# Kernel tuning notes

Measured on AMD Instinct MI355X. Metric: run time of the kernel, lower is better.

Reference implementation:

```python
import jax, jax.numpy as jnp
import numpy as np

DIM = 2048            # model dim
HID = 4096            # ssm inner dim (multiple_of*round(2/3*6144))
H = 64                # n_heads
P = HID // H          # head_dim = 64
N = 128               # state_dim
G = 1                 # n_groups
K = 4                 # conv_size
Q = 128               # chunk_size
CONV_DIM = HID + 2 * G * N       # 4352
D_IN = 2 * HID + 2 * G * N + H   # 8512
EPS = 1e-5


def _causal_conv_silu(xBC, w):
    # xBC: [B,L,C], w: [C,K]; depthwise causal conv1d fused with SiLU
    kern = w.T[:, None, :]  # [K,1,C]
    y = jax.lax.conv_general_dilated(
        xBC, kern, window_strides=(1,), padding=[(K - 1, 0)],
        dimension_numbers=('NHC', 'HIO', 'NHC'),
        feature_group_count=xBC.shape[-1])
    return y * jax.nn.sigmoid(y)


def _ssm(x, W_in, conv_w, dt_bias, A_log, D, norm_w, W_out):
    Bsz, L, _ = x.shape
    zxbcdt = x @ W_in.T                       # [B,L,D_IN]
    z = zxbcdt[..., :HID]                     # gate
    xBC = zxbcdt[..., HID:HID + CONV_DIM]
    dt_raw = zxbcdt[..., HID + CONV_DIM:]     # [B,L,H]

    xBC = _causal_conv_silu(xBC, conv_w)
    xs = xBC[..., :HID].reshape(Bsz, L, H, P)
    rep = H // G
    Bh = jnp.repeat(xBC[..., HID:HID + G * N].reshape(Bsz, L, G, N), rep, axis=2)  # [B,L,H,N]
    Ch = jnp.repeat(xBC[..., HID + G * N:].reshape(Bsz, L, G, N), rep, axis=2)

    dt = jax.nn.softplus(dt_raw + dt_bias)    # [B,L,H], dt_softplus=True
    A = -jnp.exp(A_log)                       # [H]

    # ---- chunked selective scan (Mamba2 SSD), chunk size Q ----
    nc = L // Q
    a = (dt * A).reshape(Bsz, nc, Q, H)
    cum = jnp.cumsum(a, axis=2)               # inclusive within-chunk cumsum, <= 0
    xs_c = xs.reshape(Bsz, nc, Q, H, P)
    dtc = dt.reshape(Bsz, nc, Q, H)
    Bc = Bh.reshape(Bsz, nc, Q, H, N)
    Cc = Ch.reshape(Bsz, nc, Q, H, N)

    # intra-chunk (diagonal) part: Y[i] += sum_{j<=i} exp(cum_i-cum_j) dt_j (C_i.B_j) x_j
    diff = cum[:, :, :, None, :] - cum[:, :, None, :, :]     # [b,c,i,j,h]
    tril = jnp.tril(jnp.ones((Q, Q), bool))[None, None, :, :, None]
    Lmat = jnp.exp(jnp.where(tril, diff, -jnp.inf))          # causal decay matrix
    CB = jnp.einsum('bcihn,bcjhn->bcijh', Cc, Bc)
    M = CB * Lmat * dtc[:, :, None, :, :]
    Yd = jnp.einsum('bcijh,bcjhp->bcihp', M, xs_c)

    # per-chunk end state: sum_j exp(cum_last-cum_j) dt_j x_j (x) B_j
    wdec = jnp.exp(cum[:, :, -1:, :] - cum) * dtc            # [b,c,q,h]
    states = jnp.einsum('bcqh,bcqhn,bcqhp->bchpn', wdec, Bc, xs_c)
    chunk_decay = jnp.exp(cum[:, :, -1, :])                  # [b,c,h]

    # inter-chunk recurrence over nc chunks
    def step(S, inp):
        dec, st = inp                                        # [b,h], [b,h,p,n]
        return S * dec[..., None, None] + st, S              # emit state entering chunk
    S0 = jnp.zeros((Bsz, H, P, N), x.dtype)
    _, Sprev = jax.lax.scan(step, S0,
                            (chunk_decay.transpose(1, 0, 2),
                             states.transpose(1, 0, 2, 3, 4)))
    Sprev = Sprev.transpose(1, 0, 2, 3, 4)                   # [b,c,h,p,n]

    # inter-chunk (off-diagonal) contribution
    Yoff = jnp.einsum('bcqh,bcqhn,bchpn->bcqhp', jnp.exp(cum), Cc, Sprev)

    y = (Yd + Yoff).reshape(Bsz, L, H, P) + D[None, None, :, None] * xs  # skip D
    y = y.reshape(Bsz, L, HID)

    yz = y * (z * jax.nn.sigmoid(z))                         # gated: y * silu(z)
    yn = yz * jax.lax.rsqrt(jnp.mean(yz * yz, axis=-1, keepdims=True) + EPS) * norm_w
    return yn @ W_out.T


def setup_inputs() -> dict:
    key = jax.random.key(0)
    k = jax.random.split(key, 6)
    return {
        'x': jax.random.normal(k[0], (2, 4096, DIM), jnp.float32),
        'W_in': jax.random.normal(k[1], (D_IN, DIM), jnp.float32) * DIM ** -0.5,
        'conv_w': jax.random.normal(k[2], (CONV_DIM, K), jnp.float32) * K ** -0.5,
        'dt_bias': jax.random.uniform(k[3], (H,), jnp.float32, minval=0.001, maxval=0.1),
        'A_log': jnp.log(jax.random.uniform(k[4], (H,), jnp.float32, minval=1.0, maxval=16.0)),
        'D': jnp.ones((H,), jnp.float32),
        'norm_w': jnp.ones((HID,), jnp.float32),
        'W_out': jax.random.normal(k[5], (DIM, HID), jnp.float32) * HID ** -0.5,
    }


def reference(x, W_in, conv_w, dt_bias, A_log, D, norm_w, W_out):
    return _ssm(x, W_in, conv_w, dt_bias, A_log, D, norm_w, W_out)
```

## Files before the change

### kernel.cpp

```cpp
#include <hip/hip_runtime.h>
#include <hip/hip_fp16.h>
#include <math.h>

#define ROWS   8192
#define DIMK   2048
#define HIDN   4096
#define QCH    128
#define NCHUNK 32
#define CST    136
#define RST    68

typedef __attribute__((ext_vector_type(8))) short short8;
typedef __attribute__((ext_vector_type(8))) _Float16 half8;
typedef __attribute__((ext_vector_type(4))) float floatx4;

static __device__ inline unsigned short f2h(float f){
  union { _Float16 h; unsigned short u; } v; v.h = (_Float16)f; return v.u;
}
static __device__ inline float h2f(unsigned short u){
  union { unsigned short u; _Float16 h; } v; v.u = u; return (float)v.h;
}
static __device__ inline void async_cp16(const void* g, void* l){
  __builtin_amdgcn_global_load_lds((const __attribute__((address_space(1))) void*)g,
                                   (__attribute__((address_space(3))) void*)l, 16, 0, 0);
}

__global__ void k_prep(const float* __restrict__ x, const float* __restrict__ Win,
                       const float* __restrict__ Wout, unsigned short* __restrict__ xw,
                       unsigned short* __restrict__ winb, unsigned short* __restrict__ woutb){
  int blk = blockIdx.x, t = threadIdx.x;
  const float* src; unsigned short* dst; int i;
  if (blk < 16384){ src = x;    dst = xw;    i = blk * 256 + t; }
  else if (blk < 33280){ src = Win;  dst = winb;  i = (blk - 16384) * 256 + t; }
  else { src = Wout; dst = woutb; i = (blk - 33280) * 256 + t; }
  float4 v = ((const float4*)src)[i];
  unsigned long long p = (unsigned long long)f2h(v.x)
                       | ((unsigned long long)f2h(v.y) << 16)
                       | ((unsigned long long)f2h(v.z) << 32)
                       | ((unsigned long long)f2h(v.w) << 48);
  ((unsigned long long*)dst)[i] = p;
}

#define DT_KT 128
__global__ __launch_bounds__(256)
void k_dtraw(const float* __restrict__ x, const float* __restrict__ Win,
             float* __restrict__ dtraw){
  __shared__ float ws[64 * (DT_KT + 4)];
  const int t = threadIdx.x;
  const int lane = t & 63, w = t >> 6;
  const int r0 = blockIdx.x * 8;
  const int rw = __builtin_amdgcn_readfirstlane(r0 + w * 2);
  float acc0 = 0.f, acc1 = 0.f;
  for (int k0 = 0; k0 < DIMK; k0 += DT_KT){
    __syncthreads();
#pragma unroll
    for (int l = 0; l < 8; l++){
      int fidx = (l * 256 + t) * 4;
      int row = fidx >> 7, col = fidx & 127;
      *(float4*)&ws[row * 132 + col] =
          *(const float4*)&Win[(size_t)(8448 + row) * DIMK + k0 + col];
    }
    __syncthreads();
    const float* xa = x + (size_t)rw * DIMK + k0;
    const float* xb = xa + DIMK;
#pragma unroll 8
    for (int kk = 0; kk < DT_KT; kk += 4){
      float4 wv = *(const float4*)&ws[lane * 132 + kk];
      float4 va = *(const float4*)&xa[kk];
      float4 vb = *(const float4*)&xb[kk];
      acc0 += wv.x*va.x + wv.y*va.y + wv.z*va.z + wv.w*va.w;
      acc1 += wv.x*vb.x + wv.y*vb.y + wv.z*vb.z + wv.w*vb.w;
    }
  }
  dtraw[(size_t)rw * 64 + lane]       = acc0;
  dtraw[(size_t)(rw + 1) * 64 + lane] = acc1;
}

static __device__ inline unsigned ldsaddr(const void* p){
  return (unsigned)(size_t)(const __attribute__((address_space(3))) void*)p;
}
static __device__ inline floatx4 dsr128(unsigned a){
  floatx4 d;
  asm volatile("ds_read_b128 %0, %1" : "=v"(d) : "v"(a));
  return d;
}
static __device__ inline half8 as_h8(floatx4 f){
  union { floatx4 f; half8 h; } u; u.f = f; return u.h;
}

template<int KD>
__device__ inline void gemm256_core(const unsigned short* __restrict__ A,
                                    const unsigned short* __restrict__ B,
                                    int row0, int col0,
                                    unsigned short* sA, unsigned short* sB,
                                    floatx4 (&acc)[8][4], int t){
  const int lane = t & 63, wid = t >> 6;
  const int wm = wid >> 2, wn = wid & 3;
  const int quad = lane >> 4, l16 = lane & 15;
  const int srow  = t >> 3;
  const int sslot = (t & 7) ^ (srow & 7);
  constexpr int NT = KD / 64;

  auto stageA = [&](int d, int half, int kt){
    unsigned short* dst = sA + d*256*64 + half*128*64;
    const unsigned short* src = A + (size_t)(row0 + half*128) * KD + kt*64;
#pragma unroll
    for (int i = 0; i < 2; i++)
      async_cp16(src + (size_t)(i*64 + srow) * KD + sslot*8,
                 dst + ((size_t)i*512 + t)*8);
  };
  auto stageB = [&](int d, int half, int kt){
    unsigned short* dst = sB + d*256*64 + half*128*64;
    const unsigned short* src = B + (size_t)(col0 + half*128) * KD + kt*64;
#pragma unroll
    for (int i = 0; i < 2; i++)
      async_cp16(src + (size_t)(i*64 + srow) * KD + sslot*8,
                 dst + ((size_t)i*512 + t)*8);
  };

  const unsigned sAbase = ldsaddr(sA), sBbase = ldsaddr(sB);
  floatx4 af[8][2], bf[4][2];
  auto rdA = [&](unsigned base, int fr, int ks) -> floatx4 {
    return dsr128(base + 2u*(unsigned)((fr*16 + l16)*64 + (((ks*4+quad)^(l16&7))*8)));
  };
  auto rdB = [&](unsigned base, int fc, int ks) -> floatx4 {
    return dsr128(base + 2u*(unsigned)((fc*16 + l16)*64 + (((ks*4+quad)^(l16&7))*8)));
  };
  auto mmac = [&](int mh, int nh){
    __builtin_amdgcn_s_setprio(1);
#pragma unroll
    for (int mm = 0; mm < 4; mm++)
#pragma unroll
      for (int nn = 0; nn < 2; nn++)
#pragma unroll
        for (int ks = 0; ks < 2; ks++)
          acc[mh*4+mm][nh*2+nn] = __builtin_amdgcn_mfma_f32_16x16x32_f16(
              as_h8(af[mh*4+mm][ks]), as_h8(bf[nh*2+nn][ks]), acc[mh*4+mm][nh*2+nn], 0, 0, 0);
    __builtin_amdgcn_s_setprio(0);
  };

  stageA(0,0,0); stageA(0,1,0); stageB(0,0,0); stageB(0,1,0);
  stageA(1,0,1); stageA(1,1,1);
  asm volatile("s_waitcnt vmcnt(4)" ::: "memory");
  __builtin_amdgcn_s_barrier();

  for (int T = 0; T < NT; T++){
    const int cur = T & 1;
    const unsigned aAd = sAbase + 2u*(unsigned)(cur*256*64 + wm*128*64);
    const unsigned bAd = sBbase + 2u*(unsigned)(cur*256*64 + wn*64*64);
#pragma unroll
    for (int fr = 0; fr < 4; fr++)
#pragma unroll
      for (int ks = 0; ks < 2; ks++)
        af[fr][ks] = rdA(aAd, fr, ks);
#pragma unroll
    for (int fc = 0; fc < 2; fc++)
#pragma unroll
      for (int ks = 0; ks < 2; ks++)
        bf[fc][ks] = rdB(bAd, fc, ks);
    if (T + 1 < NT) stageB(cur^1, 0, T+1);
    __builtin_amdgcn_s_barrier();
    asm volatile("s_waitcnt lgkmcnt(0)" ::: "memory");
    __builtin_amdgcn_sched_barrier(0);
    mmac(0, 0);
    __builtin_amdgcn_s_barrier();
#pragma unroll
    for (int fr = 4; fr < 8; fr++)
#pragma unroll
      for (int ks = 0; ks < 2; ks++)
        af[fr][ks] = rdA(aAd, fr, ks);
    if (T + 1 < NT) stageB(cur^1, 1, T+1);
    __builtin_amdgcn_s_barrier();
    asm volatile("s_waitcnt lgkmcnt(0)" ::: "memory");
    __builtin_amdgcn_sched_barrier(0);
    mmac(1, 0);
    __builtin_amdgcn_s_barrier();
#pragma unroll
    for (int fc = 2; fc < 4; fc++)
#pragma unroll
      for (int ks = 0; ks < 2; ks++)
        bf[fc][ks] = rdB(bAd, fc, ks);
    __builtin_amdgcn_s_barrier();
    asm volatile("s_waitcnt lgkmcnt(0)" ::: "memory");
    __builtin_amdgcn_sched_barrier(0);
    mmac(0, 1);
    __builtin_amdgcn_s_barrier();
    if (T + 2 < NT){
      stageA(cur, 0, T+2); stageA(cur, 1, T+2);
      asm volatile("s_waitcnt vmcnt(4)" ::: "memory");
    } else if (T + 1 < NT){
      asm volatile("s_waitcnt vmcnt(0)" ::: "memory");
    }
    __builtin_amdgcn_s_barrier();
    mmac(1, 1);
    __builtin_amdgcn_s_barrier();
  }
}

__global__ __launch_bounds__(512, 2)
void k_gemm1(const unsigned short* __restrict__ A, const unsigned short* __restrict__ B,
             unsigned short* __restrict__ zbuf, unsigned short* __restrict__ xsraw,
             unsigned short* __restrict__ bcraw){
  __shared__ __align__(16) unsigned short sA[2*256*64];
  __shared__ __align__(16) unsigned short sB[2*256*64];
  const int t = threadIdx.x;
  int swz = (blockIdx.x % 8) * 132 + blockIdx.x / 8;
  const int row0 = (swz & 31) * 256, col0 = (swz >> 5) * 256;
  floatx4 acc[8][4] = {};
  gemm256_core<DIMK>(A, B, row0, col0, sA, sB, acc, t);
  const int lane = t & 63, wid = t >> 6;
  const int wm = wid >> 2, wn = wid & 3;
  const int quad = lane >> 4, l16 = lane & 15;
  unsigned short* dst; int cbase, ldd;
  if (col0 < 4096){ dst = zbuf; cbase = 0; ldd = 4096; }
  else if (col0 < 8192){ dst = xsraw; cbase = 4096; ldd = 4096; }
  else { dst = bcraw; cbase = 8192; ldd = 256; }
#pragma unroll
  for (int m = 0; m < 8; m++)
#pragma unroll
    for (int n = 0; n < 4; n++){
      int rb = row0 + wm*128 + m*16 + quad*4;
      int cc = col0 + wn*64 + n*16 + l16 - cbase;
#pragma unroll
      for (int r = 0; r < 4; r++)
        dst[(size_t)(rb + r) * ldd + cc] = f2h(acc[m][n][r]);
    }
}

__global__ __launch_bounds__(512, 2)
void k_gemm2(const unsigned short* __restrict__ A, const unsigned short* __restrict__ B,
             float* __restrict__ C){
  __shared__ __align__(16) unsigned short sA[2*256*64];
  __shared__ __align__(16) unsigned short sB[2*256*64];
  const int t = threadIdx.x;
  int swz = (blockIdx.x % 8) * 32 + blockIdx.x / 8;
  const int row0 = (swz & 31) * 256, col0 = (swz >> 5) * 256;
  floatx4 acc[8][4] = {};
  gemm256_core<HIDN>(A, B, row0, col0, sA, sB, acc, t);
  const int lane = t & 63, wid = t >> 6;
  const int wm = wid >> 2, wn = wid & 3;
  const int quad = lane >> 4, l16 = lane & 15;
#pragma unroll
  for (int m = 0; m < 8; m++)
#pragma unroll
    for (int n = 0; n < 4; n++){
      int rb = row0 + wm*128 + m*16 + quad*4;
      int cc = col0 + wn*64 + n*16 + l16;
#pragma unroll
      for (int r = 0; r < 4; r++)
        C[(size_t)(rb + r) * DIMK + cc] = acc[m][n][r];
    }
}

__global__ void k_mid(const unsigned short* __restrict__ bcraw, const float* __restrict__ cw,
                      unsigned short* __restrict__ bcc,
                      const unsigned short* __restrict__ xsraw, unsigned short* __restrict__ halo,
                      const float* __restrict__ dtraw, const float* __restrict__ dtbias,
                      const float* __restrict__ Alog, float* __restrict__ dtb,
                      float* __restrict__ cumb){
  int blk = blockIdx.x, t = threadIdx.x;
  if (blk < 8192){
    int row = blk, c = t;
    int tl = row & 4095;
    const float4 wv = *(const float4*)&cw[(size_t)(4096 + c) * 4];
    const unsigned short* col = bcraw + c;
    size_t rb = (size_t)row * 256;
    float a = h2f(col[rb]) * wv.w;
    if (tl >= 1) a += h2f(col[rb - 256]) * wv.z;
    if (tl >= 2) a += h2f(col[rb - 512]) * wv.y;
    if (tl >= 3) a += h2f(col[rb - 768]) * wv.x;
    bcc[rb + c] = f2h(a / (1.f + __expf(-a)));
  } else if (blk < 11264){
    int idx = blk - 8192;
    int col = (idx & 15) * 256 + t;
    int slot = (idx >> 4) % 3;
    int bc = idx / 48;
    long r = (long)bc * QCH - 3 + slot;
    if (r >= 0)
      halo[((size_t)bc * 3 + slot) * 4096 + col] = xsraw[(size_t)r * 4096 + col];
  } else {
    int lb = blk - 11264;
    int bc = lb * 4 + (t >> 6);
    int h = t & 63;
    float bias = dtbias[h];
    float A = -__expf(Alog[h]);
    float run = 0.f;
    size_t rowb = (size_t)bc * QCH;
    for (int q = 0; q < QCH; q++){
      float dr = dtraw[(rowb + q) * 64 + h] + bias;
      float dt = dr > 20.f ? dr : log1pf(__expf(dr));
      dtb[(rowb + q) * 64 + h] = dt;
      run += dt * A;
      cumb[(rowb + q) * 64 + h] = run;
    }
  }
}

__global__ __launch_bounds__(256, 2)
void k_chunk1(const unsigned short* __restrict__ xsc, const unsigned short* __restrict__ bcc,
              const float* __restrict__ dtb, const float* __restrict__ cumb,
              const float* __restrict__ Dp, const unsigned short* __restrict__ st,
              unsigned short* __restrict__ ybuf){
  __shared__ __align__(16) unsigned short Ml[128*CST];
  __shared__ __align__(16) unsigned short xsT[64*CST];
  __shared__ float cum_s[128], dt_s[128];
  const int blk = blockIdx.x, h = blk & 63, bc = blk >> 6;
  const size_t rowb = (size_t)bc * QCH;
  const int t = threadIdx.x, w = t >> 6, lane = t & 63, quad = lane >> 4, l16 = lane & 15;
  const int wrow = w * 32;
  if (t < 128){ cum_s[t] = cumb[(rowb + t)*64 + h]; dt_s[t] = dtb[(rowb + t)*64 + h]; }
  __syncthreads();
#pragma unroll
  for (int it = 0; it < 2; it++){
    int idx = it * 256 + t;
    int q = idx & 127, p0 = (idx >> 7) * 16;
    const unsigned short* cur = xsc + (rowb + q) * 4096 + h * 64 + p0;
    short8 c0 = *(const short8*)cur, c1 = *(const short8*)(cur + 8);
#pragma unroll
    for (int j = 0; j < 16; j++)
      xsT[(p0 + j) * CST + q] = (unsigned short)(j < 8 ? c0[j] : c1[j-8]);
  }
  floatx4 acc[2][8] = {};
  const unsigned short* Cb = bcc + rowb * 256 + 128;
  const unsigned short* Bb = bcc + rowb * 256;
#pragma unroll
  for (int ks = 0; ks < 4; ks++){
    half8 af[2];
#pragma unroll
    for (int i = 0; i < 2; i++)
      af[i] = *(const half8*)(Cb + (size_t)(wrow + i*16 + l16) * 256 + ks*32 + quad*8);
#pragma unroll
    for (int j = 0; j < 8; j++){
      half8 bfr = *(const half8*)(Bb + (size_t)(j*16 + l16) * 256 + ks*32 + quad*8);
#pragma unroll
      for (int i = 0; i < 2; i++)
        acc[i][j] = __builtin_amdgcn_mfma_f32_16x16x32_f16(af[i], bfr, acc[i][j], 0, 0, 0);
    }
  }
#pragma unroll
  for (int i = 0; i < 2; i++)
#pragma unroll
    for (int j = 0; j < 8; j++){
      int jc = j*16 + l16;
      float dtj = dt_s[jc], cj = cum_s[jc];
#pragma unroll
      for (int r = 0; r < 4; r++){
        int ir = wrow + i*16 + quad*4 + r;
        float m = (ir >= jc) ? acc[i][j][r] * __expf(cum_s[ir] - cj) * dtj : 0.f;
        Ml[ir * CST + jc] = f2h(m);
      }
    }
  __syncthreads();
  floatx4 accY[2][4] = {};
#pragma unroll
  for (int ks = 0; ks < 4; ks++){
    half8 af[2], bfr[4];
#pragma unroll
    for (int i = 0; i < 2; i++)
      af[i] = *(const half8*)&Ml[(wrow + i*16 + l16)*CST + ks*32 + quad*8];
#pragma unroll
    for (int p = 0; p < 4; p++)
      bfr[p] = *(const half8*)&xsT[(p*16 + l16)*CST + ks*32 + quad*8];
#pragma unroll
    for (int i = 0; i < 2; i++)
#pragma unroll
      for (int p = 0; p < 4; p++)
        accY[i][p] = __builtin_amdgcn_mfma_f32_16x16x32_f16(af[i], bfr[p], accY[i][p], 0, 0, 0);
  }
  __syncthreads();
  unsigned short* Sp = Ml;
  {
    size_t base = ((size_t)bc * 64 + h) * 8192;
#pragma unroll
    for (int it = 0; it < 4; it++){
      int flat = it * 256 + t;
      int row = flat >> 4, col = (flat & 15) * 8;
      *(short8*)&Sp[row * CST + col] = *(const short8*)&st[base + (size_t)row * 128 + col];
    }
  }
  __syncthreads();
  floatx4 accO[2][4] = {};
#pragma unroll
  for (int ks = 0; ks < 4; ks++){
    half8 af[2], bfr[4];
#pragma unroll
    for (int i = 0; i < 2; i++)
      af[i] = *(const half8*)(Cb + (size_t)(wrow + i*16 + l16) * 256 + ks*32 + quad*8);
#pragma unroll
    for (int p = 0; p < 4; p++)
      bfr[p] = *(const half8*)&Sp[(p*16 + l16)*CST + ks*32 + quad*8];
#pragma unroll
    for (int i = 0; i < 2; i++)
#pragma unroll
      for (int p = 0; p < 4; p++)
        accO[i][p] = __builtin_amdgcn_mfma_f32_16x16x32_f16(af[i], bfr[p], accO[i][p], 0, 0, 0);
  }
  float Dh = Dp[h];
#pragma unroll
  for (int i = 0; i < 2; i++)
#pragma unroll
    for (int p = 0; p < 4; p++){
      int pc = p*16 + l16;
#pragma unroll
      for (int r = 0; r < 4; r++){
        int ir = wrow + i*16 + quad*4 + r;
        float y = accY[i][p][r] + __expf(cum_s[ir]) * accO[i][p][r] + Dh * h2f(xsT[pc*CST + ir]);
        ybuf[(rowb + ir) * (size_t)HIDN + h*64 + pc] = f2h(y);
      }
    }
}

__global__ __launch_bounds__(256, 2)
void k_chunk2(unsigned short* __restrict__ xsraw, const unsigned short* __restrict__ bcc,
              const unsigned short* __restrict__ halo, const float* __restrict__ cw,
              const float* __restrict__ dtb, const float* __restrict__ cumb,
              unsigned short* __restrict__ st){
  __shared__ __align__(16) unsigned short wBT[128*CST];
  __shared__ __align__(16) unsigned short xsT[64*CST];
  __shared__ __align__(16) unsigned short xsRaw[131*RST];
  __shared__ float cum_s[128], dt_s[128];
  __shared__ float cws[64*4];
  const int blk = blockIdx.x, h = blk & 63, bc = blk >> 6;
  const size_t rowb = (size_t)bc * QCH;
  const int t = threadIdx.x, w = t >> 6, lane = t & 63, quad = lane >> 4, l16 = lane & 15;
  if (t < 128){ cum_s[t] = cumb[(rowb + t)*64 + h]; dt_s[t] = dtb[(rowb + t)*64 + h]; }
  if (t < 64) *(float4*)&cws[t*4] = *(const float4*)&cw[((size_t)h*64 + t)*4];
#pragma unroll
  for (int it = 0; it < 5; it++){
    int flat = it * 256 + t;
    if (flat < 1048){
      int row = flat >> 3, c8 = (flat & 7) * 8;
      const unsigned short* src = (row < 3)
        ? halo + ((size_t)bc * 3 + row) * 4096 + h * 64 + c8
        : xsraw + (rowb + row - 3) * 4096 + h * 64 + c8;
      *(short8*)&xsRaw[row * RST + c8] = *(const short8*)src;
    }
  }
  __syncthreads();
  const int tl0 = (bc & 31) * QCH;
#pragma unroll
  for (int it = 0; it < 2; it++){
    int idx = it * 256 + t;
    int q = idx & 127, p0 = (idx >> 7) * 16;
    int tl = tl0 + q;
    int lr = q + 3;
    float f1 = (tl >= 1) ? 1.f : 0.f;
    float f2 = (tl >= 2) ? 1.f : 0.f;
    float f3 = (tl >= 3) ? 1.f : 0.f;
    short8 c0 = *(const short8*)&xsRaw[lr*RST + p0],     c1 = *(const short8*)&xsRaw[lr*RST + p0 + 8];
    short8 a0 = *(const short8*)&xsRaw[(lr-1)*RST + p0], a1 = *(const short8*)&xsRaw[(lr-1)*RST + p0 + 8];
    short8 b0 = *(const short8*)&xsRaw[(lr-2)*RST + p0], b1 = *(const short8*)&xsRaw[(lr-2)*RST + p0 + 8];
    short8 d0 = *(const short8*)&xsRaw[(lr-3)*RST + p0], d1 = *(const short8*)&xsRaw[(lr-3)*RST + p0 + 8];
    short8 w0, w1;
#pragma unroll
    for (int j = 0; j < 16; j++){
      int col = p0 + j;
      const float* wp = cws + col * 4;
      float vc = h2f((unsigned short)(j < 8 ? c0[j] : c1[j-8]));
      float v1 = h2f((unsigned short)(j < 8 ? a0[j] : a1[j-8]));
      float v2 = h2f((unsigned short)(j < 8 ? b0[j] : b1[j-8]));
      float v3 = h2f((unsigned short)(j < 8 ? d0[j] : d1[j-8]));
      float a = vc * wp[3] + f1 * v1 * wp[2] + f2 * v2 * wp[1] + f3 * v3 * wp[0];
      float s = a / (1.f + __expf(-a));
      unsigned short hv = f2h(s);
      xsT[col * CST + q] = hv;
      if (j < 8) w0[j] = (short)hv; else w1[j-8] = (short)hv;
    }
    unsigned short* g = xsraw + (rowb + q) * 4096 + h * 64 + p0;
    *(short8*)g = w0;
    *(short8*)(g + 8) = w1;
  }
  float clast = cum_s[127];
#pragma unroll
  for (int it = 0; it < 2; it++){
    int idx = it * 256 + t;
    int q = idx & 127, n0 = (idx >> 7) * 32;
    float wd = __expf(clast - cum_s[q]) * dt_s[q];
    const unsigned short* gp = bcc + (rowb + q) * 256 + n0;
#pragma unroll
    for (int c4 = 0; c4 < 4; c4++){
      short8 v = *(const short8*)(gp + c4*8);
#pragma unroll
      for (int jj = 0; jj < 8; jj++)
        wBT[(n0 + c4*8 + jj)*CST + q] = f2h(h2f((unsigned short)v[jj]) * wd);
    }
  }
  __syncthreads();
  floatx4 acc[8] = {};
#pragma unroll
  for (int ks = 0; ks < 4; ks++){
    half8 af = *(const half8*)&xsT[(w*16 + l16)*CST + ks*32 + quad*8];
#pragma unroll
    for (int j = 0; j < 8; j++){
      half8 bfr = *(const half8*)&wBT[(j*16 + l16)*CST + ks*32 + quad*8];
      acc[j] = __builtin_amdgcn_mfma_f32_16x16x32_f16(af, bfr, acc[j], 0, 0, 0);
    }
  }
  size_t base = ((size_t)bc * 64 + h) * 8192;
#pragma unroll
  for (int j = 0; j < 8; j++){
    int n = j*16 + l16;
#pragma unroll
    for (int r = 0; r < 4; r++){
      int p = w*16 + quad*4 + r;
      st[base + p*128 + n] = f2h(acc[j][r]);
    }
  }
}

__global__ void k_scan(unsigned short* __restrict__ st, const float* __restrict__ cumb){
  int id = blockIdx.x * 256 + threadIdx.x;
  int n2 = id & 63, p = (id >> 6) & 63, h = (id >> 12) & 63, b = id >> 18;
  float S0 = 0.f, S1 = 0.f;
  for (int c = 0; c < NCHUNK; c++){
    int bc = b * NCHUNK + c;
    size_t idx = ((size_t)bc * 64 + h) * 8192 + (size_t)p * 128 + n2 * 2;
    float dec = __expf(cumb[((size_t)bc * QCH + 127) * 64 + h]);
    unsigned v = *(const unsigned*)&st[idx];
    float v0 = h2f((unsigned short)(v & 0xffff));
    float v1 = h2f((unsigned short)(v >> 16));
    unsigned o = (unsigned)f2h(S0) | ((unsigned)f2h(S1) << 16);
    *(unsigned*)&st[idx] = o;
    S0 = S0 * dec + v0;
    S1 = S1 * dec + v1;
  }
}

__global__ __launch_bounds__(256)
void k_gate(unsigned short* __restrict__ yb, const unsigned short* __restrict__ zb,
            const float* __restrict__ nw){
  __shared__ float red[4];
  int row = blockIdx.x, t = threadIdx.x;
  size_t base = (size_t)row * HIDN + t * 16;
  short8 y0 = *(const short8*)&yb[base], y1 = *(const short8*)&yb[base + 8];
  short8 z0 = *(const short8*)&zb[base], z1 = *(const short8*)&zb[base + 8];
  float vals[16], ss = 0.f;
#pragma unroll
  for (int j = 0; j < 8; j++){
    float y = h2f((unsigned short)y0[j]);
    float z = h2f((unsigned short)z0[j]);
    float v = y * (z / (1.f + __expf(-z)));
    vals[j] = v; ss += v * v;
  }
#pragma unroll
  for (int j = 0; j < 8; j++){
    float y = h2f((unsigned short)y1[j]);
    float z = h2f((unsigned short)z1[j]);
    float v = y * (z / (1.f + __expf(-z)));
    vals[8 + j] = v; ss += v * v;
  }
  for (int o = 32; o > 0; o >>= 1) ss += __shfl_down(ss, o, 64);
  int w = t >> 6, lane = t & 63;
  if (lane == 0) red[w] = ss;
  __syncthreads();
  float scale = rsqrtf((red[0] + red[1] + red[2] + red[3]) / (float)HIDN + 1e-5f);
  const float4 nw0 = *(const float4*)&nw[t*16];
  const float4 nw1 = *(const float4*)&nw[t*16 + 4];
  const float4 nw2 = *(const float4*)&nw[t*16 + 8];
  const float4 nw3 = *(const float4*)&nw[t*16 + 12];
  float nwv[16] = { nw0.x, nw0.y, nw0.z, nw0.w, nw1.x, nw1.y, nw1.z, nw1.w,
                    nw2.x, nw2.y, nw2.z, nw2.w, nw3.x, nw3.y, nw3.z, nw3.w };
  short8 o0, o1;
#pragma unroll
  for (int j = 0; j < 8; j++){
    o0[j] = (short)f2h(vals[j] * scale * nwv[j]);
    o1[j] = (short)f2h(vals[8 + j] * scale * nwv[8 + j]);
  }
  *(short8*)&yb[base]     = o0;
  *(short8*)&yb[base + 8] = o1;
}

extern "C" void kernel_launch(void* const* d_in, const int* in_sizes, int n_in,
                              void* d_out, int out_size, void* d_ws, size_t ws_size,
                              hipStream_t stream){
  const float* x      = (const float*)d_in[0];
  const float* Win    = (const float*)d_in[1];
  const float* convw  = (const float*)d_in[2];
  const float* dtbias = (const float*)d_in[3];
  const float* Alog   = (const float*)d_in[4];
  const float* Dp     = (const float*)d_in[5];
  const float* nw     = (const float*)d_in[6];
  const float* Wout   = (const float*)d_in[7];
  float* out = (float*)d_out;

  char* ws = (char*)d_ws;
  size_t off = 0;
  auto alloc = [&](size_t bytes)->void*{ void* p = ws + off; off += (bytes + 255) & ~(size_t)255; return p; };
  unsigned short* xw    = (unsigned short*)alloc((size_t)ROWS * DIMK * 2);
  unsigned short* winb  = (unsigned short*)alloc((size_t)8448 * DIMK * 2);
  float*          dtraw = (float*)alloc((size_t)ROWS * 64 * 4);
  unsigned short* woutb = (unsigned short*)alloc((size_t)DIMK * HIDN * 2);
  unsigned short* zbuf  = (unsigned short*)alloc((size_t)ROWS * HIDN * 2);
  unsigned short* xsraw = (unsigned short*)alloc((size_t)ROWS * HIDN * 2);
  unsigned short* bcraw = (unsigned short*)alloc((size_t)ROWS * 256 * 2);
  unsigned short* bcc   = (unsigned short*)alloc((size_t)ROWS * 256 * 2);
  unsigned short* halo  = (unsigned short*)alloc((size_t)64 * 3 * 4096 * 2);
  float*          dtb   = (float*)alloc((size_t)ROWS * 64 * 4);
  float*          cumb  = (float*)alloc((size_t)ROWS * 64 * 4);
  unsigned short* st    = xw;
  unsigned short* ybuf  = xsraw;

  k_prep<<<41472, 256, 0, stream>>>(x, Win, Wout, xw, winb, woutb);
  k_dtraw<<<ROWS/8, 256, 0, stream>>>(x, Win, dtraw);
  k_gemm1<<<dim3(33*32), 512, 0, stream>>>(xw, winb, zbuf, xsraw, bcraw);
  k_mid<<<11280, 256, 0, stream>>>(bcraw, convw, bcc, xsraw, halo,
                                   dtraw, dtbias, Alog, dtb, cumb);
  k_chunk2<<<4096, 256, 0, stream>>>(xsraw, bcc, halo, convw, dtb, cumb, st);
  k_scan<<<2048, 256, 0, stream>>>(st, cumb);
  k_chunk1<<<4096, 256, 0, stream>>>(xsraw, bcc, dtb, cumb, Dp, st, ybuf);
  k_gate<<<ROWS, 256, 0, stream>>>(ybuf, zbuf, nw);
  k_gemm2<<<dim3(8*32), 512, 0, stream>>>(ybuf, woutb, out);
}
```

Measured before the change: 1.044 ms.

## Split B/C projection into separate 128-tile GEMM and stage chunk output via LDS

The first GEMM launched 33x32 tiles of 256x256, and the last tile column (B/C projection, 256 wide) formed a ragged tail wave. That column now goes to a new 128x128-tile kernel with a simple single-buffered loop, so the main GEMM runs exactly 1024 tiles. Separately, k_chunk1 now writes its y outputs to LDS first, then stores 16-byte coalesced rows to global instead of scattered 2-byte stores. The extra launch and the unpipelined small GEMM add overhead, and reusing the Ml LDS buffer needs the added barriers.

```diff
diff --git a/kernel.cpp b/kernel.cpp
--- a/kernel.cpp
+++ b/kernel.cpp
@@ -197,24 +197,60 @@
   }
 }
 
+__device__ inline void gemm128_core(const unsigned short* __restrict__ A,
+                                    const unsigned short* __restrict__ B,
+                                    int Kd, int row0, int col0,
+                                    unsigned short* lA, unsigned short* lB,
+                                    floatx4 (&acc)[4][4], int t){
+  const int w = t >> 6, lane = t & 63;
+  const int quad = lane >> 4, l16 = lane & 15;
+  const int wr = (w >> 1) * 64, wc = (w & 1) * 64;
+  for (int k0 = 0; k0 < Kd; k0 += 64){
+#pragma unroll
+    for (int i = 0; i < 4; i++){
+      int cb = i * 256 + w * 64, c = cb + lane;
+      async_cp16(A + (size_t)(row0 + (c >> 3)) * Kd + k0 + (c & 7) * 8, lA + (size_t)cb * 8);
+    }
+#pragma unroll
+    for (int i = 0; i < 4; i++){
+      int cb = i * 256 + w * 64, c = cb + lane;
+      async_cp16(B + (size_t)(col0 + (c >> 3)) * Kd + k0 + (c & 7) * 8, lB + (size_t)cb * 8);
+    }
+    __syncthreads();
+#pragma unroll
+    for (int ks = 0; ks < 2; ks++){
+      half8 af[4], bfr[4];
+#pragma unroll
+      for (int i = 0; i < 4; i++){
+        af[i]  = *(const half8*)&lA[(wr + i*16 + l16)*64 + ks*32 + quad*8];
+        bfr[i] = *(const half8*)&lB[(wc + i*16 + l16)*64 + ks*32 + quad*8];
+      }
+#pragma unroll
+      for (int i = 0; i < 4; i++)
+#pragma unroll
+        for (int j = 0; j < 4; j++)
+          acc[i][j] = __builtin_amdgcn_mfma_f32_16x16x32_f16(af[i], bfr[j], acc[i][j], 0, 0, 0);
+    }
+    __syncthreads();
+  }
+}
+
 __global__ __launch_bounds__(512, 2)
 void k_gemm1(const unsigned short* __restrict__ A, const unsigned short* __restrict__ B,
-             unsigned short* __restrict__ zbuf, unsigned short* __restrict__ xsraw,
-             unsigned short* __restrict__ bcraw){
+             unsigned short* __restrict__ zbuf, unsigned short* __restrict__ xsraw){
   __shared__ __align__(16) unsigned short sA[2*256*64];
   __shared__ __align__(16) unsigned short sB[2*256*64];
   const int t = threadIdx.x;
-  int swz = (blockIdx.x % 8) * 132 + blockIdx.x / 8;
+  int swz = (blockIdx.x % 8) * 128 + blockIdx.x / 8;
   const int row0 = (swz & 31) * 256, col0 = (swz >> 5) * 256;
   floatx4 acc[8][4] = {};
   gemm256_core<DIMK>(A, B, row0, col0, sA, sB, acc, t);
   const int lane = t & 63, wid = t >> 6;
   const int wm = wid >> 2, wn = wid & 3;
   const int quad = lane >> 4, l16 = lane & 15;
-  unsigned short* dst; int cbase, ldd;
-  if (col0 < 4096){ dst = zbuf; cbase = 0; ldd = 4096; }
-  else if (col0 < 8192){ dst = xsraw; cbase = 4096; ldd = 4096; }
-  else { dst = bcraw; cbase = 8192; ldd = 256; }
+  unsigned short* dst; int cbase;
+  if (col0 < 4096){ dst = zbuf; cbase = 0; }
+  else { dst = xsraw; cbase = 4096; }
 #pragma unroll
   for (int m = 0; m < 8; m++)
 #pragma unroll
@@ -223,7 +259,30 @@
       int cc = col0 + wn*64 + n*16 + l16 - cbase;
 #pragma unroll
       for (int r = 0; r < 4; r++)
-        dst[(size_t)(rb + r) * ldd + cc] = f2h(acc[m][n][r]);
+        dst[(size_t)(rb + r) * 4096 + cc] = f2h(acc[m][n][r]);
+    }
+}
+
+__global__ __launch_bounds__(256, 2)
+void k_gemm1bc(const unsigned short* __restrict__ A, const unsigned short* __restrict__ B,
+               unsigned short* __restrict__ bcraw){
+  __shared__ __align__(16) unsigned short lA[128*64];
+  __shared__ __align__(16) unsigned short lB[128*64];
+  const int t = threadIdx.x;
+  const int row0 = blockIdx.y * 128, col0 = 8192 + blockIdx.x * 128;
+  floatx4 acc[4][4] = {};
+  gemm128_core(A, B, DIMK, row0, col0, lA, lB, acc, t);
+  const int w = t >> 6, lane = t & 63, quad = lane >> 4, l16 = lane & 15;
+  const int wr = (w >> 1) * 64, wc = (w & 1) * 64;
+#pragma unroll
+  for (int i = 0; i < 4; i++)
+#pragma unroll
+    for (int j = 0; j < 4; j++){
+      int rb = row0 + wr + i*16 + quad*4;
+      int cc = col0 + wc + j*16 + l16 - 8192;
+#pragma unroll
+      for (int r = 0; r < 4; r++)
+        bcraw[(size_t)(rb + r) * 256 + cc] = f2h(acc[i][j][r]);
     }
 }
 
@@ -395,6 +454,8 @@
       for (int p = 0; p < 4; p++)
         accO[i][p] = __builtin_amdgcn_mfma_f32_16x16x32_f16(af[i], bfr[p], accO[i][p], 0, 0, 0);
   }
+  __syncthreads();
+  unsigned short* yl = Ml;
   float Dh = Dp[h];
 #pragma unroll
   for (int i = 0; i < 2; i++)
@@ -405,9 +466,17 @@
       for (int r = 0; r < 4; r++){
         int ir = wrow + i*16 + quad*4 + r;
         float y = accY[i][p][r] + __expf(cum_s[ir]) * accO[i][p][r] + Dh * h2f(xsT[pc*CST + ir]);
-        ybuf[(rowb + ir) * (size_t)HIDN + h*64 + pc] = f2h(y);
+        yl[ir * 68 + pc] = f2h(y);
       }
     }
+  __syncthreads();
+#pragma unroll
+  for (int it = 0; it < 4; it++){
+    int flat = it * 256 + t;
+    int row = flat >> 3, slot = (flat & 7) * 8;
+    short8 v = *(const short8*)&yl[row * 68 + slot];
+    *(short8*)&ybuf[(rowb + row) * (size_t)HIDN + h*64 + slot] = v;
+  }
 }
 
 __global__ __launch_bounds__(256, 2)
@@ -602,7 +671,8 @@
 
   k_prep<<<41472, 256, 0, stream>>>(x, Win, Wout, xw, winb, woutb);
   k_dtraw<<<ROWS/8, 256, 0, stream>>>(x, Win, dtraw);
-  k_gemm1<<<dim3(33*32), 512, 0, stream>>>(xw, winb, zbuf, xsraw, bcraw);
+  k_gemm1<<<dim3(1024), 512, 0, stream>>>(xw, winb, zbuf, xsraw);
+  k_gemm1bc<<<dim3(2, 64), 256, 0, stream>>>(xw, winb, bcraw);
   k_mid<<<11280, 256, 0, stream>>>(bcraw, convw, bcc, xsraw, halo,
                                    dtraw, dtbias, Alog, dtb, cumb);
   k_chunk2<<<4096, 256, 0, stream>>>(xsraw, bcc, halo, convw, dtb, cumb, st);
```

New measurement: 1.058 ms. About the same (+1.4%).
